# Kernel optimization log

Hardware: AMD Instinct MI355X
Metric: run time of the kernel (lower is better)

Reference implementation:

```python
import jax, jax.numpy as jnp
import numpy as np

N = 50000      # nodes
E = 1600000    # edges
IN = 128       # in_dim
HID = 128      # hidden_dim
H = 8          # heads
C = HID // H   # out_channels per head
ED = 32        # edge_feat_dim
EPS = 1e-5


def layer_norm(x, g, b):
    mu = x.mean(-1, keepdims=True)
    var = ((x - mu) ** 2).mean(-1, keepdims=True)
    return (x - mu) * jax.lax.rsqrt(var + EPS) * g + b


def setup_inputs() -> dict:
    key = jax.random.key(0)
    ks = jax.random.split(key, 24)
    w = lambda k, s, sc=0.05: (jax.random.normal(k, s, jnp.float32) * sc)
    return dict(
        x=jax.random.normal(ks[0], (N, IN), jnp.float32),
        edge_index=jax.random.randint(ks[1], (2, E), 0, N),
        edge_feats=jax.random.normal(ks[2], (E, ED), jnp.float32),
        # TransformerConv params
        Wq=w(ks[3], (IN, HID)), bq=jnp.zeros((HID,), jnp.float32),
        Wk=w(ks[4], (IN, HID)), bk=jnp.zeros((HID,), jnp.float32),
        Wv=w(ks[5], (IN, HID)), bv=jnp.zeros((HID,), jnp.float32),
        We=w(ks[6], (ED, HID)), be=jnp.zeros((HID,), jnp.float32),
        Wskip=w(ks[7], (IN, HID)), bskip=jnp.zeros((HID,), jnp.float32),
        Wbeta=w(ks[8], (3 * HID, 1)),
        ln1_g=jnp.ones((HID,), jnp.float32), ln1_b=jnp.zeros((HID,), jnp.float32),
        # GlobalContextLayer params
        Wr=w(ks[9], (HID, HID)), br=jnp.zeros((HID,), jnp.float32),
        Ww=w(ks[10], (HID, HID)), bw=jnp.zeros((HID,), jnp.float32),
        Wg=w(ks[11], (2 * HID, HID)), bg=jnp.zeros((HID,), jnp.float32),
        ln2_g=jnp.ones((HID,), jnp.float32), ln2_b=jnp.zeros((HID,), jnp.float32),
    )


def reference(x, edge_index, edge_feats,
              Wq, bq, Wk, bk, Wv, bv, We, be, Wskip, bskip, Wbeta,
              ln1_g, ln1_b, Wr, br, Ww, bw, Wg, bg, ln2_g, ln2_b):
    src, dst = edge_index[0], edge_index[1]  # messages flow src -> dst
    q = (x @ Wq + bq).reshape(N, H, C)
    k = (x @ Wk + bk).reshape(N, H, C)
    v = (x @ Wv + bv).reshape(N, H, C)
    e = (edge_feats @ We + be).reshape(E, H, C)

    k_e = k[src] + e                                   # [E,H,C]
    alpha = (q[dst] * k_e).sum(-1) / jnp.sqrt(jnp.float32(C))  # [E,H]
    # segment softmax over incoming edges of each dst node
    m = jax.ops.segment_max(alpha, dst, num_segments=N)        # [N,H]
    ex = jnp.exp(alpha - m[dst])
    s = jax.ops.segment_sum(ex, dst, num_segments=N)
    alpha = ex / (s[dst] + 1e-16)                      # [E,H]

    msg = (v[src] + e) * alpha[..., None]              # [E,H,C]
    out = jax.ops.segment_sum(msg, dst, num_segments=N).reshape(N, HID)

    # beta skip connection
    x_r = x @ Wskip + bskip
    beta = jax.nn.sigmoid(jnp.concatenate([out, x_r, out - x_r], -1) @ Wbeta)  # [N,1]
    out = beta * x_r + (1.0 - beta) * out

    # block: relu(LN(dropout(out) + residual)); dropout=0, residual_proj=None
    h = jax.nn.relu(layer_norm(out + x, ln1_g, ln1_b))

    # GlobalContextLayer
    g = jax.nn.relu(h.mean(0) @ Wr + br)               # [HID]
    g_bc = g @ Ww + bw                                 # [HID], broadcast to all nodes
    gate = jax.nn.sigmoid(jnp.concatenate([h, jnp.broadcast_to(g_bc, h.shape)], -1) @ Wg + bg)
    return layer_norm(h + gate * g_bc, ln2_g, ln2_b)
```

## Files before the change

kernel.cpp:

```cpp
#include <hip/hip_runtime.h>
#include <hip/hip_fp16.h>

#define NN 50000
#define EE 1600000
#define NB_HIST 1024
#define NB_PROJ 1563
#define NB_SCAN 49

typedef float f4v __attribute__((ext_vector_type(4)));
typedef float f2v __attribute__((ext_vector_type(2)));
typedef __attribute__((ext_vector_type(8))) short bf16x8;
typedef __attribute__((ext_vector_type(4))) float f32x4;

static __device__ __forceinline__ float4 f4z() { return make_float4(0.f, 0.f, 0.f, 0.f); }

static __device__ __forceinline__ unsigned short f2bf(float f)
{
    unsigned u = __float_as_uint(f);
    u += 0x7FFF + ((u >> 16) & 1);
    return (unsigned short)(u >> 16);
}


__global__ __launch_bounds__(256) void wpack_kernel(
    const float* __restrict__ Wq, const float* __restrict__ Wk,
    const float* __restrict__ Wv, const float* __restrict__ Ws,
    unsigned short* __restrict__ wp)
{
    int idx = blockIdx.x * 256 + threadIdx.x;
    if (idx >= 8192) return;
    int l = idx & 63;
    int t = (idx >> 6) & 7;
    int s = (idx >> 9) & 3;
    int w = idx >> 11;
    const float* W = (w == 0) ? Wq : (w == 1) ? Wk : (w == 2) ? Wv : Ws;
    int n = t * 16 + (l & 15);
    int kb = s * 32 + (l >> 4) * 8;
    union { unsigned short u16[8]; uint4 v4; } u;
    #pragma unroll
    for (int j = 0; j < 8; ++j) u.u16[j] = f2bf(W[(kb + j) * 128 + n]);
    ((uint4*)wp)[idx] = u.v4;
}


__global__ __launch_bounds__(1024) void scan1_kernel(const int* __restrict__ counts,
                                                     int* __restrict__ offsets,
                                                     int* __restrict__ bsum)
{
    __shared__ int wsum[16];
    __shared__ int wpre[16];
    const int t = threadIdx.x;
    const int lane = t & 63, wid = t >> 6;
    const int i = blockIdx.x * 1024 + t;
    int orig = (i < NN) ? counts[i] : 0;
    int val = orig;
    #pragma unroll
    for (int ofs = 1; ofs < 64; ofs <<= 1) {
        int n = __shfl_up(val, ofs);
        if (lane >= ofs) val += n;
    }
    if (lane == 63) wsum[wid] = val;
    __syncthreads();
    if (t < 16) {
        int w = wsum[t];
        #pragma unroll
        for (int ofs = 1; ofs < 16; ofs <<= 1) {
            int n = __shfl_up(w, ofs);
            if (t >= ofs) w += n;
        }
        wpre[t] = w;
    }
    __syncthreads();
    int incl = val + (wid ? wpre[wid - 1] : 0);
    if (i < NN) offsets[i] = incl - orig;
    if (t == 1023) bsum[blockIdx.x] = incl;
}

__global__ __launch_bounds__(64) void scan2_kernel(int* __restrict__ bsum,
                                                   int* __restrict__ bpre)
{
    const int t = threadIdx.x;
    int orig = (t < NB_SCAN) ? bsum[t] : 0;
    int val = orig;
    #pragma unroll
    for (int ofs = 1; ofs < 64; ofs <<= 1) {
        int n = __shfl_up(val, ofs);
        if (t >= ofs) val += n;
    }
    if (t < NB_SCAN) bpre[t] = val - orig;
}

__global__ __launch_bounds__(1024) void scan3_kernel(int* __restrict__ offsets,
                                                     int* __restrict__ cursor,
                                                     const int* __restrict__ bpre)
{
    const int i = blockIdx.x * 1024 + threadIdx.x;
    const int add = bpre[blockIdx.x];
    if (i < NN) {
        int off = offsets[i] + add;
        offsets[i] = off;
        cursor[i] = off;
    } else if (i == NN) {
        offsets[NN] = EE;
    }
}


__global__ __launch_bounds__(256) void scatter_kernel(const int* __restrict__ ei,
                                                      int* __restrict__ cursor,
                                                      int2* __restrict__ sorted2)
{
    int i = blockIdx.x * blockDim.x + threadIdx.x;
    int stride = gridDim.x * blockDim.x;
    for (; i < EE; i += stride) {
        int srcn = ei[i];
        int d = ei[EE + i];
        int pos = atomicAdd(&cursor[d], 1);
        sorted2[pos] = make_int2(i, srcn);
    }
    if (blockIdx.x == 0 && threadIdx.x < 32) sorted2[EE + threadIdx.x] = make_int2(0, 0);
}


__global__ __launch_bounds__(256) void k1_kernel(
    const int* __restrict__ ei, int* __restrict__ counts,
    const float* __restrict__ x,
    const unsigned short* __restrict__ wp,
    const float* __restrict__ bq, const float* __restrict__ bk,
    const float* __restrict__ bv, const float* __restrict__ bs,
    const float* __restrict__ We, const float* __restrict__ be,
    float* __restrict__ q, unsigned char* __restrict__ kvf8,
    float* __restrict__ xr, unsigned char* __restrict__ qef8,
    float* __restrict__ nqbe)
{
    const int tid = threadIdx.x;
    if (blockIdx.x < NB_HIST) {
        int i = blockIdx.x * 256 + tid;
        int stride = NB_HIST * 256;
        for (; i < EE; i += stride) atomicAdd(&counts[ei[EE + i]], 1);
        return;
    }
    __shared__ unsigned short xsb[32][136];
    __shared__ float qs[32][132];
    __shared__ float ksf[32][128];
    __shared__ float vsf[32][128];

    const int row0 = (blockIdx.x - NB_HIST) * 32;

    for (int i = tid; i < 1024; i += 256) {
        int r = i >> 5, c4 = i & 31;
        int gr = row0 + r;
        float4 val = f4z();
        if (gr < NN) val = ((const float4*)(x + (size_t)gr * 128))[c4];
        union { unsigned short u16[4]; uint2 v; } u;
        u.u16[0] = f2bf(val.x); u.u16[1] = f2bf(val.y);
        u.u16[2] = f2bf(val.z); u.u16[3] = f2bf(val.w);
        *(uint2*)&xsb[r][c4 * 4] = u.v;
    }
    __syncthreads();

    const int lane = tid & 63;
    const int w = tid >> 6;
    const int lr = (lane >> 4) * 4;
    const int lc = lane & 15;

    f32x4 acc[2][8];
    #pragma unroll
    for (int mt = 0; mt < 2; ++mt)
        #pragma unroll
        for (int t = 0; t < 8; ++t)
            acc[mt][t] = (f32x4){0.f, 0.f, 0.f, 0.f};

    const bf16x8* wp8 = (const bf16x8*)wp;
    #pragma unroll
    for (int s = 0; s < 4; ++s) {
        bf16x8 a0 = *(const bf16x8*)&xsb[lc][s * 32 + (lane >> 4) * 8];
        bf16x8 a1 = *(const bf16x8*)&xsb[16 + lc][s * 32 + (lane >> 4) * 8];
        #pragma unroll
        for (int t = 0; t < 8; ++t) {
            bf16x8 b = wp8[((w * 4 + s) * 8 + t) * 64 + lane];
            acc[0][t] = __builtin_amdgcn_mfma_f32_16x16x32_bf16(a0, b, acc[0][t], 0, 0, 0);
            acc[1][t] = __builtin_amdgcn_mfma_f32_16x16x32_bf16(a1, b, acc[1][t], 0, 0, 0);
        }
    }

    const float* bias = (w == 0) ? bq : (w == 1) ? bk : (w == 2) ? bv : bs;
    float bc[8];
    #pragma unroll
    for (int t = 0; t < 8; ++t) bc[t] = bias[t * 16 + lc];

    if (w == 0) {
        #pragma unroll
        for (int mt = 0; mt < 2; ++mt)
            #pragma unroll
            for (int t = 0; t < 8; ++t)
                #pragma unroll
                for (int i = 0; i < 4; ++i)
                    qs[mt * 16 + lr + i][t * 16 + lc] = acc[mt][t][i] + bc[t];
    } else if (w == 1) {
        #pragma unroll
        for (int mt = 0; mt < 2; ++mt)
            #pragma unroll
            for (int t = 0; t < 8; ++t)
                #pragma unroll
                for (int i = 0; i < 4; ++i)
                    ksf[mt * 16 + lr + i][t * 16 + lc] = acc[mt][t][i] + bc[t];
    } else if (w == 2) {
        #pragma unroll
        for (int mt = 0; mt < 2; ++mt)
            #pragma unroll
            for (int t = 0; t < 8; ++t)
                #pragma unroll
                for (int i = 0; i < 4; ++i)
                    vsf[mt * 16 + lr + i][t * 16 + lc] = acc[mt][t][i] + bc[t];
    } else {
        #pragma unroll
        for (int mt = 0; mt < 2; ++mt)
            #pragma unroll
            for (int t = 0; t < 8; ++t)
                #pragma unroll
                for (int i = 0; i < 4; ++i) {
                    int gr = row0 + mt * 16 + lr + i;
                    if (gr < NN) xr[(size_t)gr * 128 + t * 16 + lc] = acc[mt][t][i] + bc[t];
                }
    }
    __syncthreads();

    for (int i = tid; i < 1024; i += 256) {
        int r = i >> 5, c4 = i & 31;
        int gr = row0 + r;
        if (gr >= NN) continue;
        float4 qv = make_float4(qs[r][4 * c4], qs[r][4 * c4 + 1],
                                qs[r][4 * c4 + 2], qs[r][4 * c4 + 3]);
        ((float4*)(q + (size_t)gr * 128))[c4] = qv;
        float k0 = ksf[r][4 * c4 + 0], v0 = vsf[r][4 * c4 + 0];
        float k1 = ksf[r][4 * c4 + 1], v1 = vsf[r][4 * c4 + 1];
        float k2 = ksf[r][4 * c4 + 2], v2 = vsf[r][4 * c4 + 2];
        float k3 = ksf[r][4 * c4 + 3], v3 = vsf[r][4 * c4 + 3];
        int lo = 0, hi = 0;
        lo = __builtin_amdgcn_cvt_pk_fp8_f32(k0, v0, lo, false);
        lo = __builtin_amdgcn_cvt_pk_fp8_f32(k1, v1, lo, true);
        hi = __builtin_amdgcn_cvt_pk_fp8_f32(k2, v2, hi, false);
        hi = __builtin_amdgcn_cvt_pk_fp8_f32(k3, v3, hi, true);
        *(uint2*)(kvf8 + (size_t)gr * 256 + 8 * c4) = make_uint2((unsigned)lo, (unsigned)hi);
    }

    const int row = tid >> 3;
    const int j = tid & 7;
    const int gr2 = row0 + row;
    if (gr2 < NN) {
        const float* xrow = qs[row];
        #pragma unroll
        for (int hh = 0; hh < 8; ++hh) {
            float a0 = 0.f, a1 = 0.f, a2 = 0.f, a3 = 0.f;
            #pragma unroll
            for (int cc = 0; cc < 4; ++cc) {
                float4 xv = *(const float4*)&xrow[hh * 16 + 4 * cc];
                float4 w0 = *(const float4*)&We[(j * 4 + 0) * 128 + hh * 16 + 4 * cc];
                float4 w1 = *(const float4*)&We[(j * 4 + 1) * 128 + hh * 16 + 4 * cc];
                float4 w2 = *(const float4*)&We[(j * 4 + 2) * 128 + hh * 16 + 4 * cc];
                float4 w3 = *(const float4*)&We[(j * 4 + 3) * 128 + hh * 16 + 4 * cc];
                a0 += xv.x * w0.x + xv.y * w0.y + xv.z * w0.z + xv.w * w0.w;
                a1 += xv.x * w1.x + xv.y * w1.y + xv.z * w1.z + xv.w * w1.w;
                a2 += xv.x * w2.x + xv.y * w2.y + xv.z * w2.z + xv.w * w2.w;
                a3 += xv.x * w3.x + xv.y * w3.y + xv.z * w3.z + xv.w * w3.w;
            }
            int pw = 0;
            pw = __builtin_amdgcn_cvt_pk_fp8_f32(a0, a1, pw, false);
            pw = __builtin_amdgcn_cvt_pk_fp8_f32(a2, a3, pw, true);
            *(unsigned*)(qef8 + (size_t)gr2 * 256 + hh * 32 + j * 4) = (unsigned)pw;
        }
        float qb = 0.f;
        #pragma unroll
        for (int c = 0; c < 16; ++c) qb += xrow[j * 16 + c] * be[j * 16 + c];
        nqbe[(size_t)gr2 * 8 + j] = qb * 0.25f;
    }
}


__global__ __launch_bounds__(256) void attn_kernel(
    const float* __restrict__ efeat,
    const float* __restrict__ We, const float* __restrict__ be,
    const float* __restrict__ q, const unsigned char* __restrict__ qef8,
    const unsigned char* __restrict__ kvf8,
    const float* __restrict__ nqbe,
    const float* __restrict__ xr, const float* __restrict__ x,
    const float* __restrict__ Wbeta,
    const float* __restrict__ ln1g, const float* __restrict__ ln1b,
    const int* __restrict__ offsets, const int2* __restrict__ sorted2,
    float* __restrict__ h, float* __restrict__ colsum)
{
    __shared__ float WeS[32][128];
    __shared__ float cs[4][128];
    const int tid = threadIdx.x;
    for (int i = tid; i < 4096; i += 256) ((float*)WeS)[i] = We[i];
    const int lane = tid & 63;
    const int wid = tid >> 6;
    const int f0 = 2 * lane;
    const int l8 = lane & 7;
    const int grp = lane & 56;

    const float be0 = be[f0], be1 = be[f0 + 1];
    const float wbo0 = Wbeta[f0],       wbo1 = Wbeta[f0 + 1];
    const float wbr0 = Wbeta[128 + f0], wbr1 = Wbeta[128 + f0 + 1];
    const float wbd0 = Wbeta[256 + f0], wbd1 = Wbeta[256 + f0 + 1];
    const float lg0 = ln1g[f0], lg1 = ln1g[f0 + 1];
    const float lb0 = ln1b[f0], lb1 = ln1b[f0 + 1];

    cs[wid][f0] = 0.f; cs[wid][f0 + 1] = 0.f;
    __syncthreads();

    const int gwave = blockIdx.x * 4 + wid;
    const int nwave = gridDim.x * 4;

    for (int node = gwave; node < NN; node += nwave) {
        const int beg = offsets[node];
        const int end = offsets[node + 1];
        const float2 qv = *(const float2*)(q + (size_t)node * 128 + f0);
        const unsigned uqe = *(const unsigned*)(qef8 + (size_t)node * 256 + 4 * lane);
        f2v qe01 = __builtin_amdgcn_cvt_pk_f32_fp8((int)uqe, false);
        f2v qe23 = __builtin_amdgcn_cvt_pk_f32_fp8((int)uqe, true);
        const float4 qev = make_float4(qe01[0], qe01[1], qe23[0], qe23[1]);
        const float qbe25 = nqbe[(size_t)node * 8 + (lane >> 3)];

        float m = -1e30f, s = 0.f, a0 = 0.f, a1 = 0.f;
        float4 wef = f4z();

        if (beg < end) {
            int2 esA[8], esB[8];
            f4v efA[8], efB[8];
            unsigned kvA[8], kvB[8];

            #pragma unroll
            for (int u = 0; u < 8; ++u) esA[u] = sorted2[beg + u];
            #pragma unroll
            for (int u = 0; u < 8; ++u) {
                efA[u] = __builtin_nontemporal_load(
                    (const f4v*)(efeat + (size_t)esA[u].x * 32 + 4 * l8));
                kvA[u] = *(const unsigned*)(kvf8 + (size_t)esA[u].y * 256 + 4 * lane);
            }
            #pragma unroll
            for (int u = 0; u < 8; ++u) esB[u] = sorted2[beg + 8 + u];

            auto phase = [&](f4v (&efC)[8], unsigned (&kvC)[8],
                             f4v (&efN)[8], unsigned (&kvN)[8],
                             int2 (&idxN)[8], int2 (&idxF)[8], int t) {
                #pragma unroll
                for (int u = 0; u < 8; ++u) {
                    efN[u] = __builtin_nontemporal_load(
                        (const f4v*)(efeat + (size_t)idxN[u].x * 32 + 4 * l8));
                    kvN[u] = *(const unsigned*)(kvf8 + (size_t)idxN[u].y * 256 + 4 * lane);
                }
                #pragma unroll
                for (int u = 0; u < 8; ++u) idxF[u] = sorted2[t + 16 + u];

                const int cnt = end - t;
                float lgt[8]; float2 vfl[8];
                #pragma unroll
                for (int u = 0; u < 8; ++u) {
                    f2v k0v0 = __builtin_amdgcn_cvt_pk_f32_fp8((int)kvC[u], false);
                    f2v k1v1 = __builtin_amdgcn_cvt_pk_f32_fp8((int)kvC[u], true);
                    vfl[u] = make_float2(k0v0[1], k1v1[1]);
                    float part = qv.x * k0v0[0] + qv.y * k1v1[0]
                               + qev.x * efC[u][0] + qev.y * efC[u][1]
                               + qev.z * efC[u][2] + qev.w * efC[u][3];
                    part += __shfl_xor(part, 1);
                    part += __shfl_xor(part, 2);
                    part += __shfl_xor(part, 4);
                    lgt[u] = (u < cnt) ? (part * 0.25f + qbe25) : -1e30f;
                }
                float m01 = fmaxf(lgt[0], lgt[1]), m23 = fmaxf(lgt[2], lgt[3]);
                float m45 = fmaxf(lgt[4], lgt[5]), m67 = fmaxf(lgt[6], lgt[7]);
                float bm = fmaxf(fmaxf(m01, m23), fmaxf(m45, m67));
                float p[8];
                #pragma unroll
                for (int u = 0; u < 8; ++u) p[u] = __expf(lgt[u] - bm);
                float bsA = 0.f, bsB = 0.f, b0A = 0.f, b0B = 0.f, b1A = 0.f, b1B = 0.f;
                float4 befA = f4z(), befB = f4z();
                #pragma unroll
                for (int u = 0; u < 8; u += 2) {
                    bsA += p[u];     bsB += p[u + 1];
                    b0A = fmaf(p[u], vfl[u].x, b0A);        b0B = fmaf(p[u + 1], vfl[u + 1].x, b0B);
                    b1A = fmaf(p[u], vfl[u].y, b1A);        b1B = fmaf(p[u + 1], vfl[u + 1].y, b1B);
                    befA.x = fmaf(p[u], efC[u][0], befA.x); befB.x = fmaf(p[u + 1], efC[u + 1][0], befB.x);
                    befA.y = fmaf(p[u], efC[u][1], befA.y); befB.y = fmaf(p[u + 1], efC[u + 1][1], befB.y);
                    befA.z = fmaf(p[u], efC[u][2], befA.z); befB.z = fmaf(p[u + 1], efC[u + 1][2], befB.z);
                    befA.w = fmaf(p[u], efC[u][3], befA.w); befB.w = fmaf(p[u + 1], efC[u + 1][3], befB.w);
                }
                const float nm = fmaxf(m, bm);
                const float so = __expf(m - nm);
                const float sn = __expf(bm - nm);
                s  = s  * so + (bsA + bsB) * sn;
                a0 = a0 * so + (b0A + b0B) * sn;
                a1 = a1 * so + (b1A + b1B) * sn;
                wef.x = wef.x * so + (befA.x + befB.x) * sn;
                wef.y = wef.y * so + (befA.y + befB.y) * sn;
                wef.z = wef.z * so + (befA.z + befB.z) * sn;
                wef.w = wef.w * so + (befA.w + befB.w) * sn;
                m = nm;
            };

            int t = beg;
            while (true) {
                phase(efA, kvA, efB, kvB, esB, esA, t); t += 8; if (t >= end) break;
                phase(efB, kvB, efA, kvA, esA, esB, t); t += 8; if (t >= end) break;
            }
        }

        const float inv = 1.f / (s + 1e-16f);
        float o0 = fmaf(a0, inv, be0);
        float o1 = fmaf(a1, inv, be1);
        float wn0 = wef.x * inv, wn1 = wef.y * inv, wn2 = wef.z * inv, wn3 = wef.w * inv;
        float ew0 = 0.f, ew1 = 0.f;
        #pragma unroll
        for (int l2 = 0; l2 < 8; ++l2) {
            float b0 = __shfl(wn0, grp + l2);
            float b1 = __shfl(wn1, grp + l2);
            float b2 = __shfl(wn2, grp + l2);
            float b3 = __shfl(wn3, grp + l2);
            float2 w0 = *(const float2*)&WeS[4 * l2 + 0][f0];
            float2 w1 = *(const float2*)&WeS[4 * l2 + 1][f0];
            float2 w2 = *(const float2*)&WeS[4 * l2 + 2][f0];
            float2 w3 = *(const float2*)&WeS[4 * l2 + 3][f0];
            ew0 += b0 * w0.x + b1 * w1.x + b2 * w2.x + b3 * w3.x;
            ew1 += b0 * w0.y + b1 * w1.y + b2 * w2.y + b3 * w3.y;
        }
        o0 += ew0; o1 += ew1;
        if (end == beg) { o0 = 0.f; o1 = 0.f; }

        const float2 xrv = *(const float2*)(xr + (size_t)node * 128 + f0);
        float bp = o0 * wbo0 + o1 * wbo1 + xrv.x * wbr0 + xrv.y * wbr1
                 + (o0 - xrv.x) * wbd0 + (o1 - xrv.y) * wbd1;
        #pragma unroll
        for (int msk = 1; msk < 64; msk <<= 1) bp += __shfl_xor(bp, msk);
        const float beta = 1.f / (1.f + __expf(-bp));
        const float2 xv = *(const float2*)(x + (size_t)node * 128 + f0);
        float t0 = beta * xrv.x + (1.f - beta) * o0 + xv.x;
        float t1 = beta * xrv.y + (1.f - beta) * o1 + xv.y;
        float sm = t0 + t1, sq = t0 * t0 + t1 * t1;
        #pragma unroll
        for (int msk = 1; msk < 64; msk <<= 1) { sm += __shfl_xor(sm, msk); sq += __shfl_xor(sq, msk); }
        const float mu = sm * (1.f / 128.f);
        const float var = sq * (1.f / 128.f) - mu * mu;
        const float rstd = rsqrtf(var + 1e-5f);
        const float h0 = fmaxf((t0 - mu) * rstd * lg0 + lb0, 0.f);
        const float h1 = fmaxf((t1 - mu) * rstd * lg1 + lb1, 0.f);
        *(float2*)(h + (size_t)node * 128 + f0) = make_float2(h0, h1);
        cs[wid][f0] += h0; cs[wid][f0 + 1] += h1;
    }
    __syncthreads();
    if (wid == 0) {
        float c0 = cs[0][f0] + cs[1][f0] + cs[2][f0] + cs[3][f0];
        float c1 = cs[0][f0 + 1] + cs[1][f0 + 1] + cs[2][f0 + 1] + cs[3][f0 + 1];
        atomicAdd(&colsum[f0], c0);
        atomicAdd(&colsum[f0 + 1], c1);
    }
}


__global__ __launch_bounds__(1024) void gctx_kernel(
    const float* __restrict__ colsum,
    const float* __restrict__ Wr, const float* __restrict__ br,
    const float* __restrict__ Ww, const float* __restrict__ bw,
    const float* __restrict__ Wg, const float* __restrict__ bg,
    float* __restrict__ gc)
{
    __shared__ float hm[128], g[128], gb[128];
    __shared__ float red[8][128];
    const int t = threadIdx.x, f = t & 127, sl = t >> 7;
    if (sl == 0) hm[f] = colsum[f] * (1.f / (float)NN);
    __syncthreads();
    float a = 0.f;
    #pragma unroll
    for (int j = 0; j < 16; ++j) { int i = sl * 16 + j; a += hm[i] * Wr[i * 128 + f]; }
    red[sl][f] = a;
    __syncthreads();
    if (sl == 0) {
        float s = br[f];
        #pragma unroll
        for (int j = 0; j < 8; ++j) s += red[j][f];
        g[f] = fmaxf(s, 0.f);
    }
    __syncthreads();
    a = 0.f;
    #pragma unroll
    for (int j = 0; j < 16; ++j) { int i = sl * 16 + j; a += g[i] * Ww[i * 128 + f]; }
    red[sl][f] = a;
    __syncthreads();
    if (sl == 0) {
        float s = bw[f];
        #pragma unroll
        for (int j = 0; j < 8; ++j) s += red[j][f];
        gb[f] = s;
        gc[f] = s;
    }
    __syncthreads();
    a = 0.f;
    #pragma unroll
    for (int j = 0; j < 16; ++j) { int i = sl * 16 + j; a += gb[i] * Wg[(128 + i) * 128 + f]; }
    red[sl][f] = a;
    __syncthreads();
    if (sl == 0) {
        float s = bg[f];
        #pragma unroll
        for (int j = 0; j < 8; ++j) s += red[j][f];
        gc[128 + f] = s;
    }
}


__global__ __launch_bounds__(256) void final_kernel(
    const float* __restrict__ h, const float* __restrict__ Wg,
    const float* __restrict__ gc,
    const float* __restrict__ ln2g, const float* __restrict__ ln2b,
    float* __restrict__ out)
{
    __shared__ float hs[32][128];
    __shared__ float ys[32][128];
    const int tid = threadIdx.x;
    const int row0 = blockIdx.x * 32;
    for (int i = tid; i < 1024; i += 256) {
        int r = i >> 5, c4 = i & 31;
        int gr = row0 + r;
        float4 val = f4z();
        if (gr < NN) val = ((const float4*)(h + (size_t)gr * 128))[c4];
        ((float4*)hs[r])[c4] = val;
    }
    __syncthreads();
    const int cg = tid & 31;
    const int rg = tid >> 5;
    float4 a[4];
    #pragma unroll
    for (int r = 0; r < 4; ++r) a[r] = f4z();
    #pragma unroll 2
    for (int kk = 0; kk < 128; ++kk) {
        float4 w4 = ((const float4*)(Wg + kk * 128))[cg];
        #pragma unroll
        for (int r = 0; r < 4; ++r) {
            float xv = hs[4 * rg + r][kk];
            a[r].x += xv * w4.x; a[r].y += xv * w4.y; a[r].z += xv * w4.z; a[r].w += xv * w4.w;
        }
    }
    const float4 gb = ((const float4*)gc)[cg];
    const float4 c2 = ((const float4*)(gc + 128))[cg];
    #pragma unroll
    for (int r = 0; r < 4; ++r) {
        int row = 4 * rg + r;
        float4 hv = ((float4*)hs[row])[cg];
        float4 y;
        float gx;
        gx = 1.f / (1.f + __expf(-(a[r].x + c2.x))); y.x = hv.x + gx * gb.x;
        gx = 1.f / (1.f + __expf(-(a[r].y + c2.y))); y.y = hv.y + gx * gb.y;
        gx = 1.f / (1.f + __expf(-(a[r].z + c2.z))); y.z = hv.z + gx * gb.z;
        gx = 1.f / (1.f + __expf(-(a[r].w + c2.w))); y.w = hv.w + gx * gb.w;
        ((float4*)ys[row])[cg] = y;
    }
    __syncthreads();
    const int lane = tid & 63;
    const int wid = tid >> 6;
    const int f0 = 2 * lane;
    const float lg0 = ln2g[f0], lg1 = ln2g[f0 + 1];
    const float lb0 = ln2b[f0], lb1 = ln2b[f0 + 1];
    for (int rr = 0; rr < 8; ++rr) {
        int row = wid * 8 + rr;
        int gr = row0 + row;
        if (gr >= NN) continue;
        float y0 = ys[row][f0], y1 = ys[row][f0 + 1];
        float sm = y0 + y1, sq = y0 * y0 + y1 * y1;
        #pragma unroll
        for (int msk = 1; msk < 64; msk <<= 1) { sm += __shfl_xor(sm, msk); sq += __shfl_xor(sq, msk); }
        float mu = sm * (1.f / 128.f);
        float var = sq * (1.f / 128.f) - mu * mu;
        float rstd = rsqrtf(var + 1e-5f);
        float o0 = (y0 - mu) * rstd * lg0 + lb0;
        float o1 = (y1 - mu) * rstd * lg1 + lb1;
        *(float2*)(out + (size_t)gr * 128 + f0) = make_float2(o0, o1);
    }
}


extern "C" void kernel_launch(void* const* d_in, const int* in_sizes, int n_in,
                              void* d_out, int out_size, void* d_ws, size_t ws_size,
                              hipStream_t stream)
{
    const float* x    = (const float*)d_in[0];
    const int*   ei   = (const int*)d_in[1];
    const float* ef   = (const float*)d_in[2];
    const float* Wq   = (const float*)d_in[3];
    const float* bq   = (const float*)d_in[4];
    const float* Wk   = (const float*)d_in[5];
    const float* bk   = (const float*)d_in[6];
    const float* Wv   = (const float*)d_in[7];
    const float* bv   = (const float*)d_in[8];
    const float* We   = (const float*)d_in[9];
    const float* be   = (const float*)d_in[10];
    const float* Wsk  = (const float*)d_in[11];
    const float* bsk  = (const float*)d_in[12];
    const float* Wbeta= (const float*)d_in[13];
    const float* g1   = (const float*)d_in[14];
    const float* b1   = (const float*)d_in[15];
    const float* Wr   = (const float*)d_in[16];
    const float* br   = (const float*)d_in[17];
    const float* Ww   = (const float*)d_in[18];
    const float* bw   = (const float*)d_in[19];
    const float* Wg   = (const float*)d_in[20];
    const float* bg   = (const float*)d_in[21];
    const float* g2   = (const float*)d_in[22];
    const float* b2   = (const float*)d_in[23];
    float* out = (float*)d_out;

    const size_t NF = (size_t)NN * 128;
    float* q      = (float*)d_ws;
    float* xr     = q + NF;
    float* h      = xr + NF;
    unsigned char* kvf8 = (unsigned char*)(h + NF);
    unsigned char* qef8 = kvf8 + (size_t)NN * 256;
    float* nqbe   = (float*)(qef8 + (size_t)NN * 256);
    float* colsum = nqbe + (size_t)NN * 8;
    float* gc     = colsum + 128;
    unsigned short* wpk = (unsigned short*)(gc + 256);
    int* counts   = (int*)(wpk + 65536);
    int* offsets  = counts + NN;
    int* cursor   = offsets + NN + 2;
    int* bsum     = cursor + NN;
    int* bpre     = bsum + 64;
    int2* sorted2 = (int2*)(bpre + 64);

    hipMemsetAsync(counts, 0, NN * sizeof(int), stream);
    hipMemsetAsync(colsum, 0, 128 * sizeof(float), stream);

    wpack_kernel<<<32, 256, 0, stream>>>(Wq, Wk, Wv, Wsk, wpk);
    k1_kernel<<<NB_HIST + NB_PROJ, 256, 0, stream>>>(ei, counts, x, wpk,
        bq, bk, bv, bsk, We, be, q, kvf8, xr, qef8, nqbe);
    scan1_kernel<<<NB_SCAN, 1024, 0, stream>>>(counts, offsets, bsum);
    scan2_kernel<<<1, 64, 0, stream>>>(bsum, bpre);
    scan3_kernel<<<NB_SCAN + 1, 1024, 0, stream>>>(offsets, cursor, bpre);
    scatter_kernel<<<2048, 256, 0, stream>>>(ei, cursor, sorted2);
    attn_kernel<<<2048, 256, 0, stream>>>(ef, We, be, q, qef8, kvf8, nqbe, xr, x, Wbeta, g1, b1,
                                          offsets, sorted2, h, colsum);
    gctx_kernel<<<1, 1024, 0, stream>>>(colsum, Wr, br, Ww, bw, Wg, bg, gc);
    final_kernel<<<(NN + 31) / 32, 256, 0, stream>>>(h, Wg, gc, g2, b2, out);
}
```

Measured before the change: 666.5 us.

## Pre-permute edge features to FP8 in dst-sorted order during scatter

The scatter kernel now reads each edge's fp32 feature row, converts it to FP8 and writes it at the edge's sorted position. It also stores only the source index instead of an (edge id, src) pair. The attention kernel then reads contiguous 4-byte FP8 feature chunks per edge in place of random 16-byte fp32 gathers, which cuts attention-side traffic and replaces scattered reads with sequential ones. The cost is an extra 51 MB of FP8 writes in scatter, done as scattered 32-byte stores, and lower precision on edge features.

```diff
diff --git a/kernel.cpp b/kernel.cpp
--- a/kernel.cpp
+++ b/kernel.cpp
@@ -107,8 +107,10 @@
 
 
 __global__ __launch_bounds__(256) void scatter_kernel(const int* __restrict__ ei,
+                                                      const float* __restrict__ ef,
                                                       int* __restrict__ cursor,
-                                                      int2* __restrict__ sorted2)
+                                                      int* __restrict__ ssrc,
+                                                      unsigned char* __restrict__ ef8)
 {
     int i = blockIdx.x * blockDim.x + threadIdx.x;
     int stride = gridDim.x * blockDim.x;
@@ -116,9 +118,27 @@
         int srcn = ei[i];
         int d = ei[EE + i];
         int pos = atomicAdd(&cursor[d], 1);
-        sorted2[pos] = make_int2(i, srcn);
-    }
-    if (blockIdx.x == 0 && threadIdx.x < 32) sorted2[EE + threadIdx.x] = make_int2(0, 0);
+        ssrc[pos] = srcn;
+        unsigned ow[8];
+        #pragma unroll
+        for (int c = 0; c < 4; ++c) {
+            f4v a = __builtin_nontemporal_load((const f4v*)(ef + (size_t)i * 32 + 8 * c));
+            f4v b = __builtin_nontemporal_load((const f4v*)(ef + (size_t)i * 32 + 8 * c + 4));
+            int w0 = 0, w1 = 0;
+            w0 = __builtin_amdgcn_cvt_pk_fp8_f32(a[0], a[1], w0, false);
+            w0 = __builtin_amdgcn_cvt_pk_fp8_f32(a[2], a[3], w0, true);
+            w1 = __builtin_amdgcn_cvt_pk_fp8_f32(b[0], b[1], w1, false);
+            w1 = __builtin_amdgcn_cvt_pk_fp8_f32(b[2], b[3], w1, true);
+            ow[2 * c] = (unsigned)w0;
+            ow[2 * c + 1] = (unsigned)w1;
+        }
+        *(uint4*)(ef8 + (size_t)pos * 32)      = make_uint4(ow[0], ow[1], ow[2], ow[3]);
+        *(uint4*)(ef8 + (size_t)pos * 32 + 16) = make_uint4(ow[4], ow[5], ow[6], ow[7]);
+    }
+    if (blockIdx.x == 0 && threadIdx.x < 32) {
+        ssrc[EE + threadIdx.x] = 0;
+        ((uint4*)(ef8 + (size_t)EE * 32))[threadIdx.x] = make_uint4(0, 0, 0, 0);
+    }
 }
 
 
@@ -279,7 +299,7 @@
 
 
 __global__ __launch_bounds__(256) void attn_kernel(
-    const float* __restrict__ efeat,
+    const unsigned char* __restrict__ ef8,
     const float* __restrict__ We, const float* __restrict__ be,
     const float* __restrict__ q, const unsigned char* __restrict__ qef8,
     const unsigned char* __restrict__ kvf8,
@@ -287,7 +307,7 @@
     const float* __restrict__ xr, const float* __restrict__ x,
     const float* __restrict__ Wbeta,
     const float* __restrict__ ln1g, const float* __restrict__ ln1b,
-    const int* __restrict__ offsets, const int2* __restrict__ sorted2,
+    const int* __restrict__ offsets, const int* __restrict__ ssrc,
     float* __restrict__ h, float* __restrict__ colsum)
 {
     __shared__ float WeS[32][128];
@@ -327,43 +347,46 @@
         float4 wef = f4z();
 
         if (beg < end) {
-            int2 esA[8], esB[8];
-            f4v efA[8], efB[8];
+            int srcA[8], srcB[8];
+            unsigned efA[8], efB[8];
             unsigned kvA[8], kvB[8];
 
             #pragma unroll
-            for (int u = 0; u < 8; ++u) esA[u] = sorted2[beg + u];
+            for (int u = 0; u < 8; ++u) srcA[u] = ssrc[beg + u];
             #pragma unroll
             for (int u = 0; u < 8; ++u) {
                 efA[u] = __builtin_nontemporal_load(
-                    (const f4v*)(efeat + (size_t)esA[u].x * 32 + 4 * l8));
-                kvA[u] = *(const unsigned*)(kvf8 + (size_t)esA[u].y * 256 + 4 * lane);
+                    (const unsigned*)(ef8 + (size_t)(beg + u) * 32 + 4 * l8));
+                kvA[u] = *(const unsigned*)(kvf8 + (size_t)srcA[u] * 256 + 4 * lane);
             }
             #pragma unroll
-            for (int u = 0; u < 8; ++u) esB[u] = sorted2[beg + 8 + u];
-
-            auto phase = [&](f4v (&efC)[8], unsigned (&kvC)[8],
-                             f4v (&efN)[8], unsigned (&kvN)[8],
-                             int2 (&idxN)[8], int2 (&idxF)[8], int t) {
+            for (int u = 0; u < 8; ++u) srcB[u] = ssrc[beg + 8 + u];
+
+            auto phase = [&](unsigned (&efC)[8], unsigned (&kvC)[8],
+                             unsigned (&efN)[8], unsigned (&kvN)[8],
+                             int (&srcN)[8], int (&srcF)[8], int t) {
                 #pragma unroll
                 for (int u = 0; u < 8; ++u) {
                     efN[u] = __builtin_nontemporal_load(
-                        (const f4v*)(efeat + (size_t)idxN[u].x * 32 + 4 * l8));
-                    kvN[u] = *(const unsigned*)(kvf8 + (size_t)idxN[u].y * 256 + 4 * lane);
+                        (const unsigned*)(ef8 + (size_t)(t + 8 + u) * 32 + 4 * l8));
+                    kvN[u] = *(const unsigned*)(kvf8 + (size_t)srcN[u] * 256 + 4 * lane);
                 }
                 #pragma unroll
-                for (int u = 0; u < 8; ++u) idxF[u] = sorted2[t + 16 + u];
+                for (int u = 0; u < 8; ++u) srcF[u] = ssrc[t + 16 + u];
 
                 const int cnt = end - t;
-                float lgt[8]; float2 vfl[8];
+                float lgt[8]; float2 vfl[8]; float4 efv[8];
                 #pragma unroll
                 for (int u = 0; u < 8; ++u) {
+                    f2v e01 = __builtin_amdgcn_cvt_pk_f32_fp8((int)efC[u], false);
+                    f2v e23 = __builtin_amdgcn_cvt_pk_f32_fp8((int)efC[u], true);
+                    efv[u] = make_float4(e01[0], e01[1], e23[0], e23[1]);
                     f2v k0v0 = __builtin_amdgcn_cvt_pk_f32_fp8((int)kvC[u], false);
                     f2v k1v1 = __builtin_amdgcn_cvt_pk_f32_fp8((int)kvC[u], true);
                     vfl[u] = make_float2(k0v0[1], k1v1[1]);
                     float part = qv.x * k0v0[0] + qv.y * k1v1[0]
-                               + qev.x * efC[u][0] + qev.y * efC[u][1]
-                               + qev.z * efC[u][2] + qev.w * efC[u][3];
+                               + qev.x * efv[u].x + qev.y * efv[u].y
+                               + qev.z * efv[u].z + qev.w * efv[u].w;
                     part += __shfl_xor(part, 1);
                     part += __shfl_xor(part, 2);
                     part += __shfl_xor(part, 4);
@@ -382,10 +405,10 @@
                     bsA += p[u];     bsB += p[u + 1];
                     b0A = fmaf(p[u], vfl[u].x, b0A);        b0B = fmaf(p[u + 1], vfl[u + 1].x, b0B);
                     b1A = fmaf(p[u], vfl[u].y, b1A);        b1B = fmaf(p[u + 1], vfl[u + 1].y, b1B);
-                    befA.x = fmaf(p[u], efC[u][0], befA.x); befB.x = fmaf(p[u + 1], efC[u + 1][0], befB.x);
-                    befA.y = fmaf(p[u], efC[u][1], befA.y); befB.y = fmaf(p[u + 1], efC[u + 1][1], befB.y);
-                    befA.z = fmaf(p[u], efC[u][2], befA.z); befB.z = fmaf(p[u + 1], efC[u + 1][2], befB.z);
-                    befA.w = fmaf(p[u], efC[u][3], befA.w); befB.w = fmaf(p[u + 1], efC[u + 1][3], befB.w);
+                    befA.x = fmaf(p[u], efv[u].x, befA.x);  befB.x = fmaf(p[u + 1], efv[u + 1].x, befB.x);
+                    befA.y = fmaf(p[u], efv[u].y, befA.y);  befB.y = fmaf(p[u + 1], efv[u + 1].y, befB.y);
+                    befA.z = fmaf(p[u], efv[u].z, befA.z);  befB.z = fmaf(p[u + 1], efv[u + 1].z, befB.z);
+                    befA.w = fmaf(p[u], efv[u].w, befA.w);  befB.w = fmaf(p[u + 1], efv[u + 1].w, befB.w);
                 }
                 const float nm = fmaxf(m, bm);
                 const float so = __expf(m - nm);
@@ -402,8 +425,8 @@
 
             int t = beg;
             while (true) {
-                phase(efA, kvA, efB, kvB, esB, esA, t); t += 8; if (t >= end) break;
-                phase(efB, kvB, efA, kvA, esA, esB, t); t += 8; if (t >= end) break;
+                phase(efA, kvA, efB, kvB, srcB, srcA, t); t += 8; if (t >= end) break;
+                phase(efB, kvB, efA, kvA, srcA, srcB, t); t += 8; if (t >= end) break;
             }
         }
 
@@ -615,7 +638,8 @@
     float* h      = xr + NF;
     unsigned char* kvf8 = (unsigned char*)(h + NF);
     unsigned char* qef8 = kvf8 + (size_t)NN * 256;
-    float* nqbe   = (float*)(qef8 + (size_t)NN * 256);
+    unsigned char* ef8  = qef8 + (size_t)NN * 256;
+    float* nqbe   = (float*)(ef8 + (size_t)(EE + 16) * 32);
     float* colsum = nqbe + (size_t)NN * 8;
     float* gc     = colsum + 128;
     unsigned short* wpk = (unsigned short*)(gc + 256);
@@ -624,7 +648,7 @@
     int* cursor   = offsets + NN + 2;
     int* bsum     = cursor + NN;
     int* bpre     = bsum + 64;
-    int2* sorted2 = (int2*)(bpre + 64);
+    int* ssrc     = bpre + 64;
 
     hipMemsetAsync(counts, 0, NN * sizeof(int), stream);
     hipMemsetAsync(colsum, 0, 128 * sizeof(float), stream);
@@ -635,9 +659,9 @@
     scan1_kernel<<<NB_SCAN, 1024, 0, stream>>>(counts, offsets, bsum);
     scan2_kernel<<<1, 64, 0, stream>>>(bsum, bpre);
     scan3_kernel<<<NB_SCAN + 1, 1024, 0, stream>>>(offsets, cursor, bpre);
-    scatter_kernel<<<2048, 256, 0, stream>>>(ei, cursor, sorted2);
-    attn_kernel<<<2048, 256, 0, stream>>>(ef, We, be, q, qef8, kvf8, nqbe, xr, x, Wbeta, g1, b1,
-                                          offsets, sorted2, h, colsum);
+    scatter_kernel<<<2048, 256, 0, stream>>>(ei, ef, cursor, ssrc, ef8);
+    attn_kernel<<<2048, 256, 0, stream>>>(ef8, We, be, q, qef8, kvf8, nqbe, xr, x, Wbeta, g1, b1,
+                                          offsets, ssrc, h, colsum);
     gctx_kernel<<<1, 1024, 0, stream>>>(colsum, Wr, br, Ww, bw, Wg, bg, gc);
     final_kernel<<<(NN + 31) / 32, 256, 0, stream>>>(h, Wg, gc, g2, b2, out);
 }
```

Measured after the change: 678.2 us. Within noise of the previous version (+1.7%).
